# Kernel tuning notes

Measured on AMD Instinct MI355X. Metric: run time of the kernel, lower is better.

Reference implementation:

```python
import jax, jax.numpy as jnp
import numpy as np
from jax import lax

DN = ('NCHW', 'OIHW', 'NCHW')  # conv dimension numbers


def setup_inputs() -> dict:
    key = jax.random.key(0)
    ks = jax.random.split(key, 3)
    B, T, C, H, W = 4, 16, 1, 64, 64
    HID = 64
    x = jax.random.normal(ks[0], (B, T, C, H, W), dtype=jnp.float32)
    # Conv2d(in+hid -> 4*hid, k=3, padding=1) weights per layer
    w0 = jax.random.normal(ks[1], (4 * HID, C + HID, 3, 3), dtype=jnp.float32) * 0.05
    b0 = jnp.zeros((4 * HID,), dtype=jnp.float32)
    w1 = jax.random.normal(ks[2], (4 * HID, HID + HID, 3, 3), dtype=jnp.float32) * 0.05
    b1 = jnp.zeros((4 * HID,), dtype=jnp.float32)
    return {"x": x, "w0": w0, "b0": b0, "w1": w1, "b1": b1}


def _cell(x_t, h_prev, c_prev, w, b, hid):
    # ConvLSTMCell: conv over [x, h], split into 4 gates, fused LSTM math
    combined = jnp.concatenate([x_t, h_prev], axis=1)  # [B, Cin+hid, H, W]
    y = lax.conv_general_dilated(combined, w, (1, 1), 'SAME', dimension_numbers=DN)
    y = y + b[None, :, None, None]
    i, f, o, g = jnp.split(y, 4, axis=1)  # each [B, hid, H, W]
    c_next = jax.nn.sigmoid(f) * c_prev + jax.nn.sigmoid(i) * jnp.tanh(g)
    h_next = jax.nn.sigmoid(o) * jnp.tanh(c_next)
    return h_next, c_next


def reference(x, w0, b0, w1, b1):
    B, T, C, H, W = x.shape
    HID = w0.shape[0] // 4
    zeros = jnp.zeros((B, HID, H, W), dtype=x.dtype)
    init = (zeros, zeros, zeros, zeros)  # (h0, c0, h1, c1)

    def step(carry, x_t):
        h0, c0, h1, c1 = carry
        h0, c0 = _cell(x_t, h0, c0, w0, b0, HID)
        h1, c1 = _cell(h0, h1, c1, w1, b1, HID)
        return (h0, c0, h1, c1), h1

    xs = jnp.transpose(x, (1, 0, 2, 3, 4))  # [T, B, C, H, W]
    _, ys = lax.scan(step, init, xs)  # ys: [T, B, HID, H, W]
    return jnp.transpose(ys, (1, 0, 2, 3, 4))  # [B, T, HID, H, W]
```

## Files before the change

kernel.cpp:

```cpp
#include <hip/hip_runtime.h>


typedef __attribute__((ext_vector_type(8))) short short8;
typedef __attribute__((ext_vector_type(4))) float float4v;
typedef unsigned short ushort_t;
typedef unsigned int uint_t;

#define HID 64
constexpr int PIX = 4096;
constexpr int HP = 72;
constexpr int PROWS = 66;
constexpr int PIMG = HP * PROWS;
constexpr int LDSW = 18;
constexpr int HALO = 324;
constexpr int SPAD = 40;
constexpr int WCHUNK = 18432;

__device__ __forceinline__ ushort_t f2b(float f) {
    uint_t u = __float_as_uint(f);
    return (ushort_t)((u + 0x7fffu + ((u >> 16) & 1u)) >> 16);
}
__device__ __forceinline__ float sigm(float x) { return 1.f / (1.f + __expf(-x)); }
__device__ __forceinline__ float tanh_fast(float x) {
    float e = __expf(2.f * x);
    return 1.f - 2.f / (e + 1.f);
}
__device__ __forceinline__ void gl_lds16(const ushort_t* g, ushort_t* l) {
    __builtin_amdgcn_global_load_lds(
        (const __attribute__((address_space(1))) unsigned int*)g,
        (__attribute__((address_space(3))) unsigned int*)l, 16, 0, 0);
}

__global__ void cvt_pad_x(const float* __restrict__ src, ushort_t* __restrict__ dst) {
    int i = blockIdx.x * 256 + threadIdx.x;
    int bt = i >> 12, p = i & 4095, y = p >> 6, xx = p & 63;
    dst[bt * PIMG + (y + 1) * HP + xx + 1] = f2b(src[i]);
}

template <int CIN, int NCH, bool L0>
__global__ void pack_w(const float* __restrict__ w, ushort_t* __restrict__ Wp, int total) {
    int e = blockIdx.x * 256 + threadIdx.x;
    if (e >= total) return;
    int j = e & 7;
    int hidL = (e >> 3) & 15;
    int g = (e >> 7) & 3;
    int cg = (e >> 9) & 3;
    int r = e >> 11;
    int tap = r % 9; r /= 9;
    int ck = r % NCH;
    int hg = r / NCH;
    int c = ck * 32 + cg * 8 + j;
    int outc = g * 64 + hg * 16 + hidL;
    int wch;
    if (L0) wch = (c < 64) ? c + 1 : (c == 64 ? 0 : -1);
    else    wch = (c < CIN) ? c : -1;
    Wp[e] = (wch >= 0) ? f2b(w[(outc * CIN + wch) * 9 + tap]) : (ushort_t)0;
}

template <int CINV>
__device__ __forceinline__ void stage_load(const ushort_t* __restrict__ srcA,
                                           const ushort_t* __restrict__ srcB,
                                           int bstrB, int ck, int b, int by, int bx,
                                           int tid, short8 (&V)[3][3]) {
#pragma unroll
    for (int jj = 0; jj < 3; ++jj) {
        int job = tid + jj * 256;
        if (job < 576) {
            int hrow = job >> 5, ch = job & 31;
            int gch = ck * 32 + ch;
            const ushort_t* p = nullptr;
            if (gch < 64)
                p = srcA + (size_t)(b * 64 + gch) * PIMG;
            else if (gch < CINV)
                p = srcB + (size_t)b * bstrB + (size_t)(gch - 64) * PIMG;
            if (p) {
                p += (by + hrow) * HP + bx;
                V[jj][0] = *(const short8*)(p);
                V[jj][1] = *(const short8*)(p + 8);
                V[jj][2] = *(const short8*)(p + 16);
            } else {
                short8 z = {};
                V[jj][0] = z; V[jj][1] = z; V[jj][2] = z;
            }
        }
    }
}

__device__ __forceinline__ void stage_write(ushort_t* __restrict__ sIn, int tid,
                                            short8 (&V)[3][3]) {
#pragma unroll
    for (int jj = 0; jj < 3; ++jj) {
        int job = tid + jj * 256;
        if (job < 576) {
            int hrow = job >> 5, ch = job & 31;
            ushort_t* dst = sIn + hrow * LDSW * SPAD + ch;
#pragma unroll
            for (int k = 0; k < 3; ++k)
#pragma unroll
                for (int ii = 0; ii < 8; ++ii) {
                    int hx = k * 8 + ii;
                    if (hx < 18) dst[hx * SPAD] = (ushort_t)V[jj][k][ii];
                }
        }
    }
}

template <int CINV, int NCH>
__global__ __launch_bounds__(256, 1) void cell_mfma(
    const ushort_t* __restrict__ srcA,
    const ushort_t* __restrict__ srcB,
    int bstrB,
    const ushort_t* __restrict__ Wp,
    const float* __restrict__ bias,
    float* __restrict__ cst,
    ushort_t* __restrict__ hnext,
    float* __restrict__ out)
{
    __shared__ __align__(16) ushort_t sIn[HALO * SPAD];
    __shared__ __align__(16) ushort_t sW[WCHUNK];

    const int tid = threadIdx.x;
    const int lane = tid & 63;
    const int wq = tid >> 6;
    const int x = lane & 15;
    const int q = lane >> 4;
    const int b = blockIdx.x >> 4;
    const int pt = blockIdx.x & 15;
    const int by = (pt >> 2) << 4, bx = (pt & 3) << 4;
    const int hg = blockIdx.y;

    float4v acc[4][4];
#pragma unroll
    for (int m = 0; m < 4; ++m) {
        float4v bv;
#pragma unroll
        for (int r = 0; r < 4; ++r) bv[r] = bias[m * 64 + hg * 16 + q * 4 + r];
#pragma unroll
        for (int nt = 0; nt < 4; ++nt) acc[m][nt] = bv;
    }

    const int abase = q * 512 + x * 8;
    int bb[4];
#pragma unroll
    for (int nt = 0; nt < 4; ++nt)
        bb[nt] = ((wq * 4 + nt) * LDSW + x) * SPAD + q * 8;

    const ushort_t* wbase = Wp + (size_t)hg * NCH * WCHUNK;

#define STAGE_W(ck)                                                          \
    {                                                                        \
        const ushort_t* wsrc = wbase + (ck) * WCHUNK;                        \
        _Pragma("unroll") for (int k = 0; k < 9; ++k)                        \
            gl_lds16(wsrc + (k * 256 + tid) * 8, &sW[(k * 256 + tid) * 8]);  \
    }

#define COMPUTE()                                                            \
    {                                                                        \
        _Pragma("unroll") for (int tap = 0; tap < 9; ++tap) {                \
            const int dy = tap / 3, dxo = tap - dy * 3;                      \
            short8 a[4];                                                     \
            const ushort_t* wp_ = sW + tap * 2048 + abase;                   \
            _Pragma("unroll") for (int m = 0; m < 4; ++m)                    \
                a[m] = *(const short8*)(wp_ + m * 128);                      \
            _Pragma("unroll") for (int nt = 0; nt < 4; ++nt) {               \
                short8 bf = *(const short8*)&sIn[bb[nt] + (dy * LDSW + dxo) * SPAD]; \
                _Pragma("unroll") for (int m = 0; m < 4; ++m)                \
                    acc[m][nt] = __builtin_amdgcn_mfma_f32_16x16x32_bf16(    \
                        a[m], bf, acc[m][nt], 0, 0, 0);                      \
            }                                                                \
        }                                                                    \
    }

    short8 VA[3][3], VB[3][3];
    stage_load<CINV>(srcA, srcB, bstrB, 0, b, by, bx, tid, VA);
#pragma unroll
    for (int ck = 0; ck < NCH; ck += 2) {
        __syncthreads();
        if (ck + 1 < NCH)
            stage_load<CINV>(srcA, srcB, bstrB, ck + 1, b, by, bx, tid, VB);
        stage_write(sIn, tid, VA);
        STAGE_W(ck);
        __syncthreads();
        COMPUTE();
        if (ck + 1 < NCH) {
            __syncthreads();
            if (ck + 2 < NCH)
                stage_load<CINV>(srcA, srcB, bstrB, ck + 2, b, by, bx, tid, VA);
            stage_write(sIn, tid, VB);
            STAGE_W(ck + 1);
            __syncthreads();
            COMPUTE();
        }
    }

#pragma unroll
    for (int nt = 0; nt < 4; ++nt) {
        int iy = by + wq * 4 + nt, ix = bx + x;
        int px = iy * 64 + ix;
#pragma unroll
        for (int r = 0; r < 4; ++r) {
            int hid = hg * 16 + q * 4 + r;
            int idx = (b * HID + hid) * PIX + px;
            float ig = sigm(acc[0][nt][r]);
            float fg = sigm(acc[1][nt][r]);
            float og = sigm(acc[2][nt][r]);
            float gg = tanh_fast(acc[3][nt][r]);
            float c = fg * cst[idx] + ig * gg;
            float h = og * tanh_fast(c);
            cst[idx] = c;
            hnext[(size_t)(b * HID + hid) * PIMG + (iy + 1) * HP + ix + 1] = f2b(h);
            if (out) out[(size_t)b * (16 * HID * PIX) + (size_t)hid * PIX + px] = h;
        }
    }
#undef STAGE_W
#undef COMPUTE
}

extern "C" void kernel_launch(void* const* d_in, const int* in_sizes, int n_in,
                              void* d_out, int out_size, void* d_ws, size_t ws_size,
                              hipStream_t stream) {
    const float* xf = (const float*)d_in[0];
    const float* w0 = (const float*)d_in[1];
    const float* b0 = (const float*)d_in[2];
    const float* w1 = (const float*)d_in[3];
    const float* b1 = (const float*)d_in[4];
    float* out = (float*)d_out;

    char* ws = (char*)d_ws;
    const size_t HBUF = (size_t)4 * HID * PIMG;
    ushort_t* h0a = (ushort_t*)ws;
    ushort_t* h0b = h0a + HBUF;
    ushort_t* h1a = h0b + HBUF;
    ushort_t* h1b = h1a + HBUF;
    ushort_t* xpad = h1b + HBUF;
    float* c0 = (float*)(xpad + (size_t)4 * 16 * PIMG);
    float* c1 = c0 + (size_t)4 * HID * PIX;
    ushort_t* Wp0 = (ushort_t*)(c1 + (size_t)4 * HID * PIX);
    ushort_t* Wp1 = Wp0 + 221184;

    size_t zbytes = (4 * HBUF + (size_t)4 * 16 * PIMG) * sizeof(ushort_t) +
                    (size_t)2 * 4 * HID * PIX * sizeof(float);
    hipMemsetAsync(d_ws, 0, zbytes, stream);

    cvt_pad_x<<<262144 / 256, 256, 0, stream>>>(xf, xpad);
    pack_w<65, 3, true><<<221184 / 256, 256, 0, stream>>>(w0, Wp0, 221184);
    pack_w<128, 4, false><<<294912 / 256, 256, 0, stream>>>(w1, Wp1, 294912);

    dim3 grid(64, 4), blk(256);
    for (int t = 0; t < 16; ++t) {
        ushort_t* h0r = (t & 1) ? h0b : h0a;
        ushort_t* h0w = (t & 1) ? h0a : h0b;
        ushort_t* h1r = (t & 1) ? h1b : h1a;
        ushort_t* h1w = (t & 1) ? h1a : h1b;
        cell_mfma<65, 3><<<grid, blk, 0, stream>>>(
            h0r, xpad + (size_t)t * PIMG, 16 * PIMG, Wp0, b0, c0, h0w, nullptr);
        cell_mfma<128, 4><<<grid, blk, 0, stream>>>(
            h0w, h1r, HID * PIMG, Wp1, b1, c1, h1w,
            out + (size_t)t * HID * PIX);
    }
}
```

Measured before the change: 728.4 us.

## Double-buffer input and weight LDS tiles to overlap staging with MFMA compute

Allocates two LDS buffers each for the input halo tile and the weight chunk. The next chunk's global loads and async weight copy are issued before computing on the current buffer, and the input is written to the alternate buffer afterwards. This leaves one barrier per chunk instead of two and hides load latency behind the MFMA work. The cost is double the LDS footprint, about 2×(25920+36864) bytes, which is acceptable at one block per CU given launch_bounds(256,1). Register pressure also rises because staged values are held across the compute.

After: 730.5 us. Within noise of the previous version (+0.3%).

```diff
diff --git a/kernel.cpp b/kernel.cpp
--- a/kernel.cpp
+++ b/kernel.cpp
@@ -12,9 +12,11 @@
 constexpr int PROWS = 66;
 constexpr int PIMG = HP * PROWS;
 constexpr int LDSW = 18;
-constexpr int HALO = 324;
+constexpr int HROWS = 18;
+constexpr int HALO = HROWS * LDSW;
 constexpr int SPAD = 40;
 constexpr int WCHUNK = 18432;
+constexpr int NJOBS = HROWS * 32;
 
 __device__ __forceinline__ ushort_t f2b(float f) {
     uint_t u = __float_as_uint(f);
@@ -65,7 +67,7 @@
 #pragma unroll
     for (int jj = 0; jj < 3; ++jj) {
         int job = tid + jj * 256;
-        if (job < 576) {
+        if (job < NJOBS) {
             int hrow = job >> 5, ch = job & 31;
             int gch = ck * 32 + ch;
             const ushort_t* p = nullptr;
@@ -91,7 +93,7 @@
 #pragma unroll
     for (int jj = 0; jj < 3; ++jj) {
         int job = tid + jj * 256;
-        if (job < 576) {
+        if (job < NJOBS) {
             int hrow = job >> 5, ch = job & 31;
             ushort_t* dst = sIn + hrow * LDSW * SPAD + ch;
 #pragma unroll
@@ -99,7 +101,7 @@
 #pragma unroll
                 for (int ii = 0; ii < 8; ++ii) {
                     int hx = k * 8 + ii;
-                    if (hx < 18) dst[hx * SPAD] = (ushort_t)V[jj][k][ii];
+                    if (hx < LDSW) dst[hx * SPAD] = (ushort_t)V[jj][k][ii];
                 }
         }
     }
@@ -116,8 +118,10 @@
     ushort_t* __restrict__ hnext,
     float* __restrict__ out)
 {
-    __shared__ __align__(16) ushort_t sIn[HALO * SPAD];
-    __shared__ __align__(16) ushort_t sW[WCHUNK];
+    __shared__ __align__(16) ushort_t sIn0[HALO * SPAD];
+    __shared__ __align__(16) ushort_t sIn1[HALO * SPAD];
+    __shared__ __align__(16) ushort_t sW0[WCHUNK];
+    __shared__ __align__(16) ushort_t sW1[WCHUNK];
 
     const int tid = threadIdx.x;
     const int lane = tid & 63;
@@ -147,23 +151,23 @@
 
     const ushort_t* wbase = Wp + (size_t)hg * NCH * WCHUNK;
 
-#define STAGE_W(ck)                                                          \
+#define STAGE_W(ck, sw)                                                      \
     {                                                                        \
         const ushort_t* wsrc = wbase + (ck) * WCHUNK;                        \
         _Pragma("unroll") for (int k = 0; k < 9; ++k)                        \
-            gl_lds16(wsrc + (k * 256 + tid) * 8, &sW[(k * 256 + tid) * 8]);  \
-    }
-
-#define COMPUTE()                                                            \
+            gl_lds16(wsrc + (k * 256 + tid) * 8, &(sw)[(k * 256 + tid) * 8]);\
+    }
+
+#define COMPUTE(si, sw)                                                      \
     {                                                                        \
         _Pragma("unroll") for (int tap = 0; tap < 9; ++tap) {                \
             const int dy = tap / 3, dxo = tap - dy * 3;                      \
             short8 a[4];                                                     \
-            const ushort_t* wp_ = sW + tap * 2048 + abase;                   \
+            const ushort_t* wp_ = (sw) + tap * 2048 + abase;                 \
             _Pragma("unroll") for (int m = 0; m < 4; ++m)                    \
                 a[m] = *(const short8*)(wp_ + m * 128);                      \
             _Pragma("unroll") for (int nt = 0; nt < 4; ++nt) {               \
-                short8 bf = *(const short8*)&sIn[bb[nt] + (dy * LDSW + dxo) * SPAD]; \
+                short8 bf = *(const short8*)&(si)[bb[nt] + (dy * LDSW + dxo) * SPAD]; \
                 _Pragma("unroll") for (int m = 0; m < 4; ++m)                \
                     acc[m][nt] = __builtin_amdgcn_mfma_f32_16x16x32_bf16(    \
                         a[m], bf, acc[m][nt], 0, 0, 0);                      \
@@ -171,26 +175,26 @@
         }                                                                    \
     }
 
-    short8 VA[3][3], VB[3][3];
-    stage_load<CINV>(srcA, srcB, bstrB, 0, b, by, bx, tid, VA);
-#pragma unroll
-    for (int ck = 0; ck < NCH; ck += 2) {
+    short8 V[3][3];
+    stage_load<CINV>(srcA, srcB, bstrB, 0, b, by, bx, tid, V);
+    STAGE_W(0, sW0);
+    stage_write(sIn0, tid, V);
+    __syncthreads();
+
+#pragma unroll
+    for (int ck = 0; ck < NCH; ++ck) {
+        ushort_t* sI  = (ck & 1) ? sIn1 : sIn0;
+        ushort_t* sWc = (ck & 1) ? sW1 : sW0;
+        ushort_t* sIa = (ck & 1) ? sIn0 : sIn1;
+        ushort_t* sWa = (ck & 1) ? sW0 : sW1;
+        if (ck + 1 < NCH) {
+            stage_load<CINV>(srcA, srcB, bstrB, ck + 1, b, by, bx, tid, V);
+            STAGE_W(ck + 1, sWa);
+        }
+        COMPUTE(sI, sWc);
+        if (ck + 1 < NCH)
+            stage_write(sIa, tid, V);
         __syncthreads();
-        if (ck + 1 < NCH)
-            stage_load<CINV>(srcA, srcB, bstrB, ck + 1, b, by, bx, tid, VB);
-        stage_write(sIn, tid, VA);
-        STAGE_W(ck);
-        __syncthreads();
-        COMPUTE();
-        if (ck + 1 < NCH) {
-            __syncthreads();
-            if (ck + 2 < NCH)
-                stage_load<CINV>(srcA, srcB, bstrB, ck + 2, b, by, bx, tid, VA);
-            stage_write(sIn, tid, VB);
-            STAGE_W(ck + 1);
-            __syncthreads();
-            COMPUTE();
-        }
     }
 
 #pragma unroll
```

## Split output channels into 8 groups and interleave gates per MFMA row

Applied to the files above, without the earlier changes.

Halves each block's output-channel slice from 16 to 8 hidden units and doubles the grid to 512 blocks, repacking weights so that each MFMA row block holds all four gates of one hidden unit. Each lane then receives i,f,o,g in its four accumulator registers. The per-block weight chunk shrinks and the launch bound is raised to allow three blocks per CU, improving occupancy and CU coverage for this small per-step problem. The cost is that every input halo tile is now loaded twice as many times across the grid, and each block issues fewer MFMAs per staged tile.

New measurement: 684.4 us. -6.0%, faster.

```diff
diff --git a/kernel.cpp b/kernel.cpp
--- a/kernel.cpp
+++ b/kernel.cpp
@@ -12,9 +12,12 @@
 constexpr int PROWS = 66;
 constexpr int PIMG = HP * PROWS;
 constexpr int LDSW = 18;
-constexpr int HALO = 324;
+constexpr int HROWS = 18;
+constexpr int HALO = HROWS * LDSW;
 constexpr int SPAD = 40;
-constexpr int WCHUNK = 18432;
+constexpr int WCHUNK = 9216;
+constexpr int W16 = WCHUNK / 8;
+constexpr int NJOBS = HROWS * 32;
 
 __device__ __forceinline__ ushort_t f2b(float f) {
     uint_t u = __float_as_uint(f);
@@ -42,15 +45,16 @@
     int e = blockIdx.x * 256 + threadIdx.x;
     if (e >= total) return;
     int j = e & 7;
-    int hidL = (e >> 3) & 15;
-    int g = (e >> 7) & 3;
-    int cg = (e >> 9) & 3;
-    int r = e >> 11;
-    int tap = r % 9; r /= 9;
-    int ck = r % NCH;
-    int hg = r / NCH;
+    int row = (e >> 3) & 15;
+    int mf = (e >> 7) & 1;
+    int cg = (e >> 8) & 3;
+    int r2 = e >> 10;
+    int tap = r2 % 9; r2 /= 9;
+    int ck = r2 % NCH;
+    int hg = r2 / NCH;
+    int hq = row >> 2, g = row & 3;
+    int outc = g * 64 + hg * 8 + mf * 4 + hq;
     int c = ck * 32 + cg * 8 + j;
-    int outc = g * 64 + hg * 16 + hidL;
     int wch;
     if (L0) wch = (c < 64) ? c + 1 : (c == 64 ? 0 : -1);
     else    wch = (c < CIN) ? c : -1;
@@ -65,7 +69,7 @@
 #pragma unroll
     for (int jj = 0; jj < 3; ++jj) {
         int job = tid + jj * 256;
-        if (job < 576) {
+        if (job < NJOBS) {
             int hrow = job >> 5, ch = job & 31;
             int gch = ck * 32 + ch;
             const ushort_t* p = nullptr;
@@ -91,7 +95,7 @@
 #pragma unroll
     for (int jj = 0; jj < 3; ++jj) {
         int job = tid + jj * 256;
-        if (job < 576) {
+        if (job < NJOBS) {
             int hrow = job >> 5, ch = job & 31;
             ushort_t* dst = sIn + hrow * LDSW * SPAD + ch;
 #pragma unroll
@@ -99,14 +103,14 @@
 #pragma unroll
                 for (int ii = 0; ii < 8; ++ii) {
                     int hx = k * 8 + ii;
-                    if (hx < 18) dst[hx * SPAD] = (ushort_t)V[jj][k][ii];
+                    if (hx < LDSW) dst[hx * SPAD] = (ushort_t)V[jj][k][ii];
                 }
         }
     }
 }
 
 template <int CINV, int NCH>
-__global__ __launch_bounds__(256, 1) void cell_mfma(
+__global__ __launch_bounds__(256, 3) void cell_mfma(
     const ushort_t* __restrict__ srcA,
     const ushort_t* __restrict__ srcB,
     int bstrB,
@@ -129,17 +133,17 @@
     const int by = (pt >> 2) << 4, bx = (pt & 3) << 4;
     const int hg = blockIdx.y;
 
-    float4v acc[4][4];
-#pragma unroll
-    for (int m = 0; m < 4; ++m) {
+    float4v acc[2][4];
+#pragma unroll
+    for (int mf = 0; mf < 2; ++mf) {
         float4v bv;
 #pragma unroll
-        for (int r = 0; r < 4; ++r) bv[r] = bias[m * 64 + hg * 16 + q * 4 + r];
-#pragma unroll
-        for (int nt = 0; nt < 4; ++nt) acc[m][nt] = bv;
-    }
-
-    const int abase = q * 512 + x * 8;
+        for (int r = 0; r < 4; ++r) bv[r] = bias[r * 64 + hg * 8 + mf * 4 + q];
+#pragma unroll
+        for (int nt = 0; nt < 4; ++nt) acc[mf][nt] = bv;
+    }
+
+    const int abase = q * 256 + x * 8;
     int bb[4];
 #pragma unroll
     for (int nt = 0; nt < 4; ++nt)
@@ -150,23 +154,26 @@
 #define STAGE_W(ck)                                                          \
     {                                                                        \
         const ushort_t* wsrc = wbase + (ck) * WCHUNK;                        \
-        _Pragma("unroll") for (int k = 0; k < 9; ++k)                        \
-            gl_lds16(wsrc + (k * 256 + tid) * 8, &sW[(k * 256 + tid) * 8]);  \
+        _Pragma("unroll") for (int k = 0; k < 5; ++k) {                      \
+            int i_ = k * 256 + tid;                                          \
+            if (i_ < W16) gl_lds16(wsrc + i_ * 8, &sW[i_ * 8]);              \
+        }                                                                    \
     }
 
 #define COMPUTE()                                                            \
     {                                                                        \
         _Pragma("unroll") for (int tap = 0; tap < 9; ++tap) {                \
             const int dy = tap / 3, dxo = tap - dy * 3;                      \
-            short8 a[4];                                                     \
-            const ushort_t* wp_ = sW + tap * 2048 + abase;                   \
-            _Pragma("unroll") for (int m = 0; m < 4; ++m)                    \
-                a[m] = *(const short8*)(wp_ + m * 128);                      \
+            short8 a[2];                                                     \
+            const ushort_t* wp_ = sW + tap * 1024 + abase;                   \
+            a[0] = *(const short8*)(wp_);                                    \
+            a[1] = *(const short8*)(wp_ + 128);                              \
             _Pragma("unroll") for (int nt = 0; nt < 4; ++nt) {               \
                 short8 bf = *(const short8*)&sIn[bb[nt] + (dy * LDSW + dxo) * SPAD]; \
-                _Pragma("unroll") for (int m = 0; m < 4; ++m)                \
-                    acc[m][nt] = __builtin_amdgcn_mfma_f32_16x16x32_bf16(    \
-                        a[m], bf, acc[m][nt], 0, 0, 0);                      \
+                acc[0][nt] = __builtin_amdgcn_mfma_f32_16x16x32_bf16(        \
+                    a[0], bf, acc[0][nt], 0, 0, 0);                          \
+                acc[1][nt] = __builtin_amdgcn_mfma_f32_16x16x32_bf16(        \
+                    a[1], bf, acc[1][nt], 0, 0, 0);                          \
             }                                                                \
         }                                                                    \
     }
@@ -198,13 +205,13 @@
         int iy = by + wq * 4 + nt, ix = bx + x;
         int px = iy * 64 + ix;
 #pragma unroll
-        for (int r = 0; r < 4; ++r) {
-            int hid = hg * 16 + q * 4 + r;
+        for (int mf = 0; mf < 2; ++mf) {
+            int hid = hg * 8 + mf * 4 + q;
             int idx = (b * HID + hid) * PIX + px;
-            float ig = sigm(acc[0][nt][r]);
-            float fg = sigm(acc[1][nt][r]);
-            float og = sigm(acc[2][nt][r]);
-            float gg = tanh_fast(acc[3][nt][r]);
+            float ig = sigm(acc[mf][nt][0]);
+            float fg = sigm(acc[mf][nt][1]);
+            float og = sigm(acc[mf][nt][2]);
+            float gg = tanh_fast(acc[mf][nt][3]);
             float c = fg * cst[idx] + ig * gg;
             float h = og * tanh_fast(c);
             cst[idx] = c;
@@ -246,7 +253,7 @@
     pack_w<65, 3, true><<<221184 / 256, 256, 0, stream>>>(w0, Wp0, 221184);
     pack_w<128, 4, false><<<294912 / 256, 256, 0, stream>>>(w1, Wp1, 294912);
 
-    dim3 grid(64, 4), blk(256);
+    dim3 grid(64, 8), blk(256);
     for (int t = 0; t < 16; ++t) {
         ushort_t* h0r = (t & 1) ? h0b : h0a;
         ushort_t* h0w = (t & 1) ? h0a : h0b;
```
